# Kernel optimization log

Measured on AMD Instinct MI355X. Metric: run time of the kernel, lower is better.

## Reference

```python
import jax, jax.numpy as jnp
import numpy as np

B, N, C, H = 8, 1024, 768, 12
HD = C // H  # 64
SCALE = HD ** -0.5
T = 4
N_HALF = T // 2  # loop body with attention runs N_HALF times, V accumulates T times


def setup_inputs() -> dict:
    key = jax.random.key(0)
    ks = jax.random.split(key, 8)
    s = 0.02
    return {
        "x": jax.random.normal(ks[0], (B, N, C), jnp.float32),
        "Wqkv": jax.random.normal(ks[1], (3 * C, C), jnp.float32) * s,
        "Wfc1": jax.random.normal(ks[2], (HD, HD), jnp.float32) * s,
        "bfc1": jax.random.normal(ks[3], (HD,), jnp.float32) * s,
        "Wfc2": jax.random.normal(ks[4], (HD, HD), jnp.float32) * s,
        "bfc2": jax.random.normal(ks[5], (HD,), jnp.float32) * s,
        "Wproj": jax.random.normal(ks[6], (C, C), jnp.float32) * s,
        "bproj": jax.random.normal(ks[7], (C,), jnp.float32) * s,
    }


def reference(x, Wqkv, Wfc1, bfc1, Wfc2, bfc2, Wproj, bproj):
    b, n, c = x.shape
    # qkv projection (no bias), split into per-head q,k,v: [B,H,N,hd]
    qkv = (x @ Wqkv.T).reshape(b, n, 3, H, HD).transpose(2, 0, 3, 1, 4)
    q, k, v = qkv[0], qkv[1], qkv[2]
    # Loop body is stateless per timestep: first N_HALF steps each add the same
    # att_spk; all T steps add the same relu(v). Compute once, scale by counts.
    Q_spk = jax.nn.relu(q) @ Wfc1.T + bfc1  # [B,H,N,hd]
    K_spk = jax.nn.relu(k) @ Wfc2.T + bfc2  # [B,H,N,hd]
    att_spk = jax.nn.relu(jnp.einsum("bhqd,bhkd->bhqk", Q_spk, K_spk) * SCALE)
    att_rec = att_spk * float(N_HALF)   # accumulated over t < T/2
    V_rec = jax.nn.relu(v) * float(T)   # accumulated over all T steps
    att = jax.nn.softmax(att_rec, axis=-1)
    out = jnp.einsum("bhqk,bhkd->bhqd", att, V_rec)  # [B,H,N,hd]
    out = out.transpose(0, 2, 1, 3).reshape(b, n, c)
    return out @ Wproj.T + bproj
```

## Files before the change

### kernel.cpp

```cpp
#include <hip/hip_runtime.h>
#include <hip/hip_bf16.h>
#include <stdint.h>
#include <math.h>

#define BB   8
#define NN_  1024
#define CC   768
#define HH   12
#define HDD  64

typedef __attribute__((ext_vector_type(8))) short bf16x8;
typedef __attribute__((ext_vector_type(4))) float f32x4;
typedef __attribute__((ext_vector_type(16))) float f32x16;
typedef __attribute__((ext_vector_type(4))) float f32x4v;
typedef __attribute__((ext_vector_type(4))) unsigned short u16x4;

union FragU { unsigned int u[4]; bf16x8 b; };

__device__ __forceinline__ unsigned short f2bf(float f) {
    union { float f; unsigned int u; } v; v.f = f;
    unsigned int r = v.u + 0x7fffu + ((v.u >> 16) & 1u);
    return (unsigned short)(r >> 16);
}

#define CVTPK(d_, a_, b_) asm("v_cvt_pk_bf16_f32 %0, %1, %2" : "=v"(d_) : "v"(a_), "v"(b_))
#define SWAP32(a_, b_) asm("v_permlane32_swap_b32 %0, %1" : "+v"(a_), "+v"(b_))

#define GLDS(g_, l_) __builtin_amdgcn_global_load_lds( \
    (const __attribute__((address_space(1))) void*)(g_), \
    (__attribute__((address_space(3))) void*)(l_), 16, 0, 0)

#define MKFRAGS(P_, F0_, F1_) do {                                             \
    unsigned int c0,c1,c2,c3,c4,c5,c6,c7;                                      \
    CVTPK(c0, P_[0],  P_[1]);  CVTPK(c1, P_[2],  P_[3]);                       \
    CVTPK(c2, P_[4],  P_[5]);  CVTPK(c3, P_[6],  P_[7]);                       \
    CVTPK(c4, P_[8],  P_[9]);  CVTPK(c5, P_[10], P_[11]);                      \
    CVTPK(c6, P_[12], P_[13]); CVTPK(c7, P_[14], P_[15]);                      \
    SWAP32(c0, c2); SWAP32(c1, c3); SWAP32(c4, c6); SWAP32(c5, c7);            \
    FragU fu0_, fu1_;                                                          \
    fu0_.u[0]=c0; fu0_.u[1]=c1; fu0_.u[2]=c2; fu0_.u[3]=c3;                    \
    fu1_.u[0]=c4; fu1_.u[1]=c5; fu1_.u[2]=c6; fu1_.u[3]=c7;                    \
    F0_ = fu0_.b; F1_ = fu1_.b;                                                \
} while (0)

#define CVT_N0 1572864
#define CVT_N1 2015232
#define CVT_N2 2162688
#define CVT_N3 2163712
#define CVT_N4 2164736
__global__ void cvt_all(const float* __restrict__ x, const float* __restrict__ wqkv,
                        const float* __restrict__ wproj, const float* __restrict__ wf1,
                        const float* __restrict__ wf2,
                        unsigned short* __restrict__ xb, unsigned short* __restrict__ wqkvb,
                        unsigned short* __restrict__ wprojb, unsigned short* __restrict__ wf1b,
                        unsigned short* __restrict__ wf2b) {
    int i = blockIdx.x * blockDim.x + threadIdx.x;
    int stride = gridDim.x * blockDim.x;
    for (; i < CVT_N4; i += stride) {
        const f32x4v* src; u16x4* dst; int off;
        if (i < CVT_N0)      { src = (const f32x4v*)x;     dst = (u16x4*)xb;     off = i; }
        else if (i < CVT_N1) { src = (const f32x4v*)wqkv;  dst = (u16x4*)wqkvb;  off = i - CVT_N0; }
        else if (i < CVT_N2) { src = (const f32x4v*)wproj; dst = (u16x4*)wprojb; off = i - CVT_N1; }
        else if (i < CVT_N3) { src = (const f32x4v*)wf1;   dst = (u16x4*)wf1b;   off = i - CVT_N2; }
        else                 { src = (const f32x4v*)wf2;   dst = (u16x4*)wf2b;   off = i - CVT_N3; }
        f32x4v v = src[off];
        u16x4 o;
        o.x = f2bf(v.x); o.y = f2bf(v.y); o.z = f2bf(v.z); o.w = f2bf(v.w);
        dst[off] = o;
    }
}

__global__ __launch_bounds__(512, 1)
void qkv_spk_gemm(const unsigned short* __restrict__ X,
                  const unsigned short* __restrict__ Wqkv,
                  const unsigned short* __restrict__ Wf1,
                  const unsigned short* __restrict__ Wf2,
                  const float* __restrict__ bf1,
                  const float* __restrict__ bf2,
                  unsigned short* __restrict__ Rq,
                  unsigned short* __restrict__ Rk,
                  unsigned short* __restrict__ VT) {
    __shared__ short sA[4][8192];
    __shared__ short sB[4][4096];

    const int t    = threadIdx.x;
    const int wid  = t >> 6;
    const int lane = t & 63;
    const int l31  = lane & 31;
    const int hi5  = lane >> 5;
    const int fw   = wid >> 1;
    const int wn   = wid & 1;

    const int bid  = (int)blockIdx.x;
    const int c    = bid & 7;
    const int j    = bid >> 3;
    const int f_   = j % 9;
    const int g_   = j / 9;
    const int bx   = c * 8 + g_;
    const int by   = f_;
    const int F0   = by * 256;
    const int T0   = bx * 128;

#define STG(bi_, kt_) do {                                                     \
    _Pragma("unroll")                                                          \
    for (int i = 0; i < 2; i++) {                                              \
        int li_ = i * 512 + t;                                                 \
        int dr_ = li_ >> 3;                                                    \
        int u_  = (li_ & 7) ^ (dr_ & 7);                                       \
        GLDS(Wqkv + (size_t)(F0 + dr_ * 2 + (u_ >> 2)) * 768 + (kt_) * 32 + (u_ & 3) * 8, \
             &sA[bi_][li_ * 8]);                                               \
    }                                                                          \
    {                                                                          \
        int dr_ = t >> 3;                                                      \
        int u_  = (t & 7) ^ (dr_ & 7);                                         \
        GLDS(X + (size_t)(T0 + dr_ * 2 + (u_ >> 2)) * 768 + (kt_) * 32 + (u_ & 3) * 8, \
             &sB[bi_][t * 8]);                                                 \
    }                                                                          \
} while (0)

    f32x16 acc[2][2];
#pragma unroll
    for (int fb = 0; fb < 2; fb++)
#pragma unroll
        for (int tb = 0; tb < 2; tb++)
#pragma unroll
            for (int r = 0; r < 16; r++) acc[fb][tb][r] = 0.f;

    bf16x8 wA[2][2], xA[2][2], wB[2][2], xB[2][2];

#define RD(W_, X_, bc_) do {                                                   \
    const char* ab_ = (const char*)sA[bc_];                                    \
    const char* bb_ = (const char*)sB[bc_];                                    \
    _Pragma("unroll")                                                          \
    for (int fb = 0; fb < 2; fb++) {                                           \
        int r_ = fw * 64 + fb * 32 + l31;                                      \
        int dr_ = r_ >> 1;                                                     \
        _Pragma("unroll")                                                      \
        for (int ks = 0; ks < 2; ks++)                                         \
            W_[fb][ks] = *(const bf16x8*)(ab_ + dr_ * 128 +                    \
                ((((r_ & 1) * 4 + ks * 2 + hi5) ^ (dr_ & 7)) << 4));           \
    }                                                                          \
    _Pragma("unroll")                                                          \
    for (int tb = 0; tb < 2; tb++) {                                           \
        int r_ = wn * 64 + tb * 32 + l31;                                      \
        int dr_ = r_ >> 1;                                                     \
        _Pragma("unroll")                                                      \
        for (int ks = 0; ks < 2; ks++)                                         \
            X_[tb][ks] = *(const bf16x8*)(bb_ + dr_ * 128 +                    \
                ((((r_ & 1) * 4 + ks * 2 + hi5) ^ (dr_ & 7)) << 4));           \
    }                                                                          \
} while (0)

#define MFMA8(W_, X_)                                                          \
    _Pragma("unroll")                                                          \
    for (int ks = 0; ks < 2; ks++)                                             \
        _Pragma("unroll")                                                      \
        for (int fb = 0; fb < 2; fb++)                                         \
            _Pragma("unroll")                                                  \
            for (int tb = 0; tb < 2; tb++)                                     \
                acc[fb][tb] = __builtin_amdgcn_mfma_f32_32x32x16_bf16(         \
                    W_[fb][ks], X_[tb][ks], acc[fb][tb], 0, 0, 0)

#define PH(CW_, CX_, NW_, NX_, rb_, sb_, t_, VM_) do {                         \
    if ((t_) + 3 < 24) STG(sb_, (t_) + 3);                                     \
    asm volatile("s_waitcnt vmcnt(" #VM_ ")" ::: "memory");                    \
    __builtin_amdgcn_s_barrier();                                              \
    if ((t_) + 1 < 24) RD(NW_, NX_, rb_);                                      \
    __builtin_amdgcn_sched_barrier(0);                                         \
    __builtin_amdgcn_s_setprio(1);                                             \
    MFMA8(CW_, CX_);                                                           \
    __builtin_amdgcn_s_setprio(0);                                             \
    asm volatile("s_waitcnt lgkmcnt(0)" ::: "memory");                         \
} while (0)

    STG(0, 0); STG(1, 1); STG(2, 2);
    asm volatile("s_waitcnt vmcnt(6)" ::: "memory");
    __builtin_amdgcn_s_barrier();
    RD(wA, xA, 0);
    asm volatile("s_waitcnt lgkmcnt(0)" ::: "memory");

#pragma unroll 1
    for (int t4 = 0; t4 < 20; t4 += 4) {
        PH(wA, xA, wB, xB, 1, 3, t4 + 0, 6);
        PH(wB, xB, wA, xA, 2, 0, t4 + 1, 6);
        PH(wA, xA, wB, xB, 3, 1, t4 + 2, 6);
        PH(wB, xB, wA, xA, 0, 2, t4 + 3, 6);
    }
    PH(wA, xA, wB, xB, 1, 3, 20, 6);
    PH(wB, xB, wA, xA, 2, 0, 21, 3);
    PH(wA, xA, wB, xB, 3, 1, 22, 0);
    PH(wB, xB, wA, xA, 0, 2, 23, 0);
#undef PH
#undef MFMA8
#undef RD
#undef STG

    const int fbase = F0 + fw * 64;
    const int p  = fbase / 768;
    const int hh = (fbase - p * 768) >> 6;
    const int tok0 = T0 + wn * 64;
    const int b  = tok0 >> 10;
    const int n0 = tok0 & 1023;
    const int crow0 = 4 * hi5;

    if (p == 2) {
        const size_t vtb = ((size_t)(b * HH + hh)) * HDD * NN_;
#pragma unroll
        for (int fb = 0; fb < 2; fb++)
#pragma unroll
            for (int tb = 0; tb < 2; tb++)
#pragma unroll
                for (int r = 0; r < 16; r++) {
                    int d = fb * 32 + (r & 3) + 8 * (r >> 2) + crow0;
                    int n = n0 + tb * 32 + l31;
                    VT[vtb + (size_t)d * NN_ + n] = f2bf(4.f * fmaxf(acc[fb][tb][r], 0.f));
                }
    } else {
        const unsigned short* Wf = p ? Wf2 : Wf1;
        const float* bfp = p ? bf2 : bf1;
        unsigned short* R = p ? Rk : Rq;
        bf16x8 wfr[2][4];
#pragma unroll
        for (int dh = 0; dh < 2; dh++)
#pragma unroll
            for (int ks = 0; ks < 4; ks++)
                wfr[dh][ks] = *(const bf16x8*)&Wf[(size_t)(dh * 32 + l31) * HDD + ks * 16 + hi5 * 8];
        float bv0 = bfp[l31], bv1 = bfp[32 + l31];
        const size_t qkb = ((size_t)(b * HH + hh)) * NN_ * HDD;
#pragma unroll
        for (int tb = 0; tb < 2; tb++) {
            float pv0[16], pv1[16];
#pragma unroll
            for (int r = 0; r < 16; r++) {
                pv0[r] = fmaxf(acc[0][tb][r], 0.f);
                pv1[r] = fmaxf(acc[1][tb][r], 0.f);
            }
            bf16x8 pa0, pa1, pa2, pa3;
            MKFRAGS(pv0, pa0, pa1);
            MKFRAGS(pv1, pa2, pa3);
            f32x16 D0, D1;
#pragma unroll
            for (int r = 0; r < 16; r++) { D0[r] = 0.f; D1[r] = 0.f; }
            D0 = __builtin_amdgcn_mfma_f32_32x32x16_bf16(pa0, wfr[0][0], D0, 0, 0, 0);
            D0 = __builtin_amdgcn_mfma_f32_32x32x16_bf16(pa1, wfr[0][1], D0, 0, 0, 0);
            D0 = __builtin_amdgcn_mfma_f32_32x32x16_bf16(pa2, wfr[0][2], D0, 0, 0, 0);
            D0 = __builtin_amdgcn_mfma_f32_32x32x16_bf16(pa3, wfr[0][3], D0, 0, 0, 0);
            D1 = __builtin_amdgcn_mfma_f32_32x32x16_bf16(pa0, wfr[1][0], D1, 0, 0, 0);
            D1 = __builtin_amdgcn_mfma_f32_32x32x16_bf16(pa1, wfr[1][1], D1, 0, 0, 0);
            D1 = __builtin_amdgcn_mfma_f32_32x32x16_bf16(pa2, wfr[1][2], D1, 0, 0, 0);
            D1 = __builtin_amdgcn_mfma_f32_32x32x16_bf16(pa3, wfr[1][3], D1, 0, 0, 0);
#pragma unroll
            for (int r = 0; r < 16; r++) {
                int n = n0 + tb * 32 + (r & 3) + 8 * (r >> 2) + crow0;
                size_t rowb = qkb + (size_t)n * HDD;
                R[rowb + l31]      = f2bf(D0[r] + bv0);
                R[rowb + 32 + l31] = f2bf(D1[r] + bv1);
            }
        }
    }
}

__global__ __launch_bounds__(256, 2)
void attn_kernel(const unsigned short* __restrict__ Q,
                 const unsigned short* __restrict__ Kx,
                 const unsigned short* __restrict__ VT,
                 unsigned short* __restrict__ AO) {
    __shared__ short sK[2][64 * 64];
    __shared__ short sV[2][64 * 64];
    __shared__ float sinv[4][32];

    const int t    = threadIdx.x;
    const int lane = t & 63;
    const int wid  = t >> 6;
    const int l31  = lane & 31;
    const int hi5  = lane >> 5;

    const int bid = (int)blockIdx.x;
    const int lbid = (bid & 7) * 96 + (bid >> 3);
    const int bh = lbid >> 3;
    const int qt = lbid & 7;
    const int b = bh / HH, h = bh - b * HH;

    const unsigned short* Qs = Q  + (size_t)bh * NN_ * HDD;
    const unsigned short* Ks = Kx + (size_t)bh * NN_ * HDD;
    const unsigned short* Vt = VT + (size_t)bh * HDD * NN_;
    const int q0 = qt * 128 + wid * 32;

    bf16x8 qf[4];
#pragma unroll
    for (int ds = 0; ds < 4; ds++)
        qf[ds] = *(const bf16x8*)&Qs[(size_t)(q0 + l31) * HDD + ds * 16 + hi5 * 8];

    f32x16 O0, O1;
#pragma unroll
    for (int r = 0; r < 16; r++) { O0[r] = 0.f; O1[r] = 0.f; }
    float sumacc = 0.f;

    const int srow = t >> 3;
    const int sslot = t & 7;
    const int dstoff = ((t & 192)) * 8;

#define STAGE(buf_, kt_) do {                                                  \
    _Pragma("unroll")                                                          \
    for (int i = 0; i < 2; i++) {                                              \
        int row_ = srow + i * 32;                                              \
        int sl_  = (sslot ^ (row_ & 7)) << 3;                                  \
        const unsigned short* gk_ = Ks + (size_t)((kt_) * 64 + row_) * HDD + sl_; \
        const unsigned short* gv_ = Vt + (size_t)row_ * NN_ + (kt_) * 64 + sl_;   \
        GLDS(gk_, &sK[buf_][i * 2048 + dstoff]);                               \
        GLDS(gv_, &sV[buf_][i * 2048 + dstoff]);                               \
    }                                                                          \
} while (0)

    STAGE(0, 0);
    __syncthreads();

    int buf = 0;
    for (int kt = 0; kt < 16; ++kt) {
        if (kt < 15) STAGE(buf ^ 1, kt + 1);

        const char* kbase = (const char*)&sK[buf][0];
        const char* vbase = (const char*)&sV[buf][0];

        bf16x8 vbf[4][2];
#pragma unroll
        for (int ks = 0; ks < 4; ks++)
#pragma unroll
            for (int dt = 0; dt < 2; dt++) {
                int d = dt * 32 + l31;
                vbf[ks][dt] = *(const bf16x8*)(vbase + d * 128 +
                               ((ks * 32 + hi5 * 16) ^ ((d & 7) << 4)));
            }
        bf16x8 ka[2][4];
#pragma unroll
        for (int kt2 = 0; kt2 < 2; kt2++)
#pragma unroll
            for (int ds = 0; ds < 4; ds++) {
                int kk = kt2 * 32 + l31;
                ka[kt2][ds] = *(const bf16x8*)(kbase + kk * 128 +
                               ((ds * 32 + hi5 * 16) ^ ((kk & 7) << 4)));
            }

        f32x16 S0, S1;
#pragma unroll
        for (int r = 0; r < 16; r++) { S0[r] = 0.f; S1[r] = 0.f; }
#pragma unroll
        for (int ds = 0; ds < 4; ds++) {
            S0 = __builtin_amdgcn_mfma_f32_32x32x16_bf16(ka[0][ds], qf[ds], S0, 0, 0, 0);
            S1 = __builtin_amdgcn_mfma_f32_32x32x16_bf16(ka[1][ds], qf[ds], S1, 0, 0, 0);
        }

        float p0[16], p1[16];
#pragma unroll
        for (int r = 0; r < 16; r++) {
            p0[r] = exp2f(0.36067376f * fmaxf(S0[r], 0.f));
            p1[r] = exp2f(0.36067376f * fmaxf(S1[r], 0.f));
        }
        float s0 = 0.f, s1 = 0.f;
#pragma unroll
        for (int r = 0; r < 16; r++) { s0 += p0[r]; s1 += p1[r]; }
        sumacc += s0 + s1;

        bf16x8 paf0, paf1, paf2, paf3;
        MKFRAGS(p0, paf0, paf1);
        MKFRAGS(p1, paf2, paf3);

        O0 = __builtin_amdgcn_mfma_f32_32x32x16_bf16(paf0, vbf[0][0], O0, 0, 0, 0);
        O1 = __builtin_amdgcn_mfma_f32_32x32x16_bf16(paf0, vbf[0][1], O1, 0, 0, 0);
        O0 = __builtin_amdgcn_mfma_f32_32x32x16_bf16(paf1, vbf[1][0], O0, 0, 0, 0);
        O1 = __builtin_amdgcn_mfma_f32_32x32x16_bf16(paf1, vbf[1][1], O1, 0, 0, 0);
        O0 = __builtin_amdgcn_mfma_f32_32x32x16_bf16(paf2, vbf[2][0], O0, 0, 0, 0);
        O1 = __builtin_amdgcn_mfma_f32_32x32x16_bf16(paf2, vbf[2][1], O1, 0, 0, 0);
        O0 = __builtin_amdgcn_mfma_f32_32x32x16_bf16(paf3, vbf[3][0], O0, 0, 0, 0);
        O1 = __builtin_amdgcn_mfma_f32_32x32x16_bf16(paf3, vbf[3][1], O1, 0, 0, 0);

        __syncthreads();
        buf ^= 1;
    }
#undef STAGE

    float stot = sumacc + __shfl_xor(sumacc, 32, 64);
    float inv = 1.f / stot;
    if (l31 == lane) sinv[wid][l31] = inv;
    __syncthreads();

#pragma unroll
    for (int r = 0; r < 16; r++) {
        int qloc = (r & 3) + 8 * (r >> 2) + 4 * hi5;
        float iv = sinv[wid][qloc];
        size_t row = (size_t)(b * NN_ + q0 + qloc) * CC + h * HDD;
        AO[row + l31]      = f2bf(O0[r] * iv);
        AO[row + 32 + l31] = f2bf(O1[r] * iv);
    }
}

__global__ __launch_bounds__(256)
void proj_gemm(const unsigned short* __restrict__ A,
               const unsigned short* __restrict__ Bt,
               const float* __restrict__ bias,
               float* __restrict__ Out) {
    __shared__ short sA[128 * 32];
    __shared__ short sB[128 * 32];
    const int K = 768;
    const int lane = threadIdx.x & 63;
    const int wid  = threadIdx.x >> 6;
    const int wr = wid >> 1, wc = wid & 1;
    const int brow = blockIdx.x * 128;
    const int bcol = blockIdx.y * 128;
    const int t = threadIdx.x;

    f32x4 acc[4][4];
#pragma unroll
    for (int m = 0; m < 4; m++)
#pragma unroll
        for (int n = 0; n < 4; n++) acc[m][n] = (f32x4){0.f, 0.f, 0.f, 0.f};

    for (int k0 = 0; k0 < K; k0 += 32) {
#pragma unroll
        for (int i = 0; i < 2; i++) {
            int tt  = i * 256 + t;
            int row = tt >> 2;
            int kc  = (tt & 3) * 8;
            const unsigned short* ga = A  + (size_t)(brow + row) * K + k0 + kc;
            const unsigned short* gb = Bt + (size_t)(bcol + row) * K + k0 + kc;
            GLDS(ga, &sA[(i * 256 + wid * 64) * 8]);
            GLDS(gb, &sB[(i * 256 + wid * 64) * 8]);
        }
        __syncthreads();
        bf16x8 af[4], bfg[4];
#pragma unroll
        for (int m = 0; m < 4; m++) {
            int r = wr * 64 + m * 16 + (lane & 15);
            af[m] = *(const bf16x8*)&sA[r * 32 + (lane >> 4) * 8];
        }
#pragma unroll
        for (int n = 0; n < 4; n++) {
            int c = wc * 64 + n * 16 + (lane & 15);
            bfg[n] = *(const bf16x8*)&sB[c * 32 + (lane >> 4) * 8];
        }
#pragma unroll
        for (int m = 0; m < 4; m++)
#pragma unroll
            for (int n = 0; n < 4; n++)
                acc[m][n] = __builtin_amdgcn_mfma_f32_16x16x32_bf16(af[m], bfg[n], acc[m][n], 0, 0, 0);
        __syncthreads();
    }
#pragma unroll
    for (int m = 0; m < 4; m++)
#pragma unroll
        for (int n = 0; n < 4; n++) {
            int col = bcol + wc * 64 + n * 16 + (lane & 15);
            float bv = bias[col];
#pragma unroll
            for (int r = 0; r < 4; r++) {
                int row = brow + wr * 64 + m * 16 + (lane >> 4) * 4 + r;
                Out[(size_t)row * 768 + col] = acc[m][n][r] + bv;
            }
        }
}

extern "C" void kernel_launch(void* const* d_in, const int* in_sizes, int n_in,
                              void* d_out, int out_size, void* d_ws, size_t ws_size,
                              hipStream_t stream) {
    const float* x     = (const float*)d_in[0];
    const float* Wqkv  = (const float*)d_in[1];
    const float* Wfc1  = (const float*)d_in[2];
    const float* bfc1  = (const float*)d_in[3];
    const float* Wfc2  = (const float*)d_in[4];
    const float* bfc2  = (const float*)d_in[5];
    const float* Wproj = (const float*)d_in[6];
    const float* bproj = (const float*)d_in[7];
    float* out = (float*)d_out;

    char* ws = (char*)d_ws;
    const size_t SZ_XN = (size_t)8192 * 768 * 2;
    unsigned short* x_bf    = (unsigned short*)ws; ws += SZ_XN;
    unsigned short* wqkv_bf = (unsigned short*)ws; ws += (size_t)2304 * 768 * 2;
    unsigned short* wproj_bf= (unsigned short*)ws; ws += (size_t)768 * 768 * 2;
    unsigned short* wfc1_bf = (unsigned short*)ws; ws += 64 * 64 * 2;
    unsigned short* wfc2_bf = (unsigned short*)ws; ws += 64 * 64 * 2;
    unsigned short* Rq      = (unsigned short*)ws; ws += SZ_XN;
    unsigned short* Rk      = (unsigned short*)ws; ws += SZ_XN;
    unsigned short* VT      = (unsigned short*)ws; ws += SZ_XN;

    cvt_all<<<2048, 256, 0, stream>>>(x, Wqkv, Wproj, Wfc1, Wfc2,
                                      x_bf, wqkv_bf, wproj_bf, wfc1_bf, wfc2_bf);
    qkv_spk_gemm<<<576, 512, 0, stream>>>(x_bf, wqkv_bf, wfc1_bf, wfc2_bf,
                                          bfc1, bfc2, Rq, Rk, VT);
    attn_kernel<<<768, 256, 0, stream>>>(Rq, Rk, VT, x_bf);
    proj_gemm<<<dim3(64, 6), 256, 0, stream>>>(x_bf, wproj_bf, bproj, out);
}
```

Baseline: 134.8 us.

## Triple-buffer attention and proj loads; stream X fragments directly from global

The QKV GEMM stops staging X tiles through LDS. Each wave now loads its X fragments straight from global memory into registers two k-steps ahead, which frees LDS, and the launch-bounds occupancy hint is raised. The attention and projection kernels move from double-buffered loops with two __syncthreads per step to 3-stage buffers with prefetch two tiles ahead and one explicit vmcnt-wait plus barrier per step. The aim is more load/compute overlap and less synchronisation, at the cost of more registers and uncoalesced direct global reads of X.

Result: slower. 235.5 us (+74.7%).

```diff
diff --git a/kernel.cpp b/kernel.cpp
--- a/kernel.cpp
+++ b/kernel.cpp
@@ -70,8 +70,8 @@
     }
 }
 
-__global__ __launch_bounds__(512, 1)
-void qkv_spk_gemm(const unsigned short* __restrict__ X,
+__global__ __launch_bounds__(512, 4)
+void qkv_spk_gemm(const unsigned short* __restrict__ Xg,
                   const unsigned short* __restrict__ Wqkv,
                   const unsigned short* __restrict__ Wf1,
                   const unsigned short* __restrict__ Wf2,
@@ -81,7 +81,6 @@
                   unsigned short* __restrict__ Rk,
                   unsigned short* __restrict__ VT) {
     __shared__ short sA[4][8192];
-    __shared__ short sB[4][4096];
 
     const int t    = threadIdx.x;
     const int wid  = t >> 6;
@@ -101,7 +100,10 @@
     const int F0   = by * 256;
     const int T0   = bx * 128;
 
-#define STG(bi_, kt_) do {                                                     \
+    const int xrow = T0 + wn * 64 + l31;
+    const int xcol8 = hi5 * 8;
+
+#define STGA(bi_, kt_) do {                                                    \
     _Pragma("unroll")                                                          \
     for (int i = 0; i < 2; i++) {                                              \
         int li_ = i * 512 + t;                                                 \
@@ -110,12 +112,15 @@
         GLDS(Wqkv + (size_t)(F0 + dr_ * 2 + (u_ >> 2)) * 768 + (kt_) * 32 + (u_ & 3) * 8, \
              &sA[bi_][li_ * 8]);                                               \
     }                                                                          \
-    {                                                                          \
-        int dr_ = t >> 3;                                                      \
-        int u_  = (t & 7) ^ (dr_ & 7);                                         \
-        GLDS(X + (size_t)(T0 + dr_ * 2 + (u_ >> 2)) * 768 + (kt_) * 32 + (u_ & 3) * 8, \
-             &sB[bi_][t * 8]);                                                 \
-    }                                                                          \
+} while (0)
+
+#define XLD(X_, kt_) do {                                                      \
+    _Pragma("unroll")                                                          \
+    for (int tb = 0; tb < 2; tb++)                                             \
+        _Pragma("unroll")                                                      \
+        for (int ks = 0; ks < 2; ks++)                                         \
+            X_[tb][ks] = *(const bf16x8*)&Xg[(size_t)(xrow + tb * 32) * 768 +  \
+                                             (kt_) * 32 + ks * 16 + xcol8];    \
 } while (0)
 
     f32x16 acc[2][2];
@@ -126,11 +131,10 @@
 #pragma unroll
             for (int r = 0; r < 16; r++) acc[fb][tb][r] = 0.f;
 
-    bf16x8 wA[2][2], xA[2][2], wB[2][2], xB[2][2];
-
-#define RD(W_, X_, bc_) do {                                                   \
+    bf16x8 wA[2][2], wB[2][2], xA[2][2], xB[2][2];
+
+#define RDA(W_, bc_) do {                                                      \
     const char* ab_ = (const char*)sA[bc_];                                    \
-    const char* bb_ = (const char*)sB[bc_];                                    \
     _Pragma("unroll")                                                          \
     for (int fb = 0; fb < 2; fb++) {                                           \
         int r_ = fw * 64 + fb * 32 + l31;                                      \
@@ -140,15 +144,6 @@
             W_[fb][ks] = *(const bf16x8*)(ab_ + dr_ * 128 +                    \
                 ((((r_ & 1) * 4 + ks * 2 + hi5) ^ (dr_ & 7)) << 4));           \
     }                                                                          \
-    _Pragma("unroll")                                                          \
-    for (int tb = 0; tb < 2; tb++) {                                           \
-        int r_ = wn * 64 + tb * 32 + l31;                                      \
-        int dr_ = r_ >> 1;                                                     \
-        _Pragma("unroll")                                                      \
-        for (int ks = 0; ks < 2; ks++)                                         \
-            X_[tb][ks] = *(const bf16x8*)(bb_ + dr_ * 128 +                    \
-                ((((r_ & 1) * 4 + ks * 2 + hi5) ^ (dr_ & 7)) << 4));           \
-    }                                                                          \
 } while (0)
 
 #define MFMA8(W_, X_)                                                          \
@@ -161,39 +156,42 @@
                 acc[fb][tb] = __builtin_amdgcn_mfma_f32_32x32x16_bf16(         \
                     W_[fb][ks], X_[tb][ks], acc[fb][tb], 0, 0, 0)
 
-#define PH(CW_, CX_, NW_, NX_, rb_, sb_, t_, VM_) do {                         \
-    if ((t_) + 3 < 24) STG(sb_, (t_) + 3);                                     \
+#define PH(CW_, CX_, NW_, rb_, sb_, t_, VM_) do {                              \
+    if ((t_) + 3 < 24) STGA(sb_, (t_) + 3);                                    \
     asm volatile("s_waitcnt vmcnt(" #VM_ ")" ::: "memory");                    \
     __builtin_amdgcn_s_barrier();                                              \
-    if ((t_) + 1 < 24) RD(NW_, NX_, rb_);                                      \
+    if ((t_) + 1 < 24) RDA(NW_, rb_);                                          \
     __builtin_amdgcn_sched_barrier(0);                                         \
     __builtin_amdgcn_s_setprio(1);                                             \
     MFMA8(CW_, CX_);                                                           \
     __builtin_amdgcn_s_setprio(0);                                             \
+    if ((t_) + 2 < 24) XLD(CX_, (t_) + 2);                                     \
     asm volatile("s_waitcnt lgkmcnt(0)" ::: "memory");                         \
 } while (0)
 
-    STG(0, 0); STG(1, 1); STG(2, 2);
-    asm volatile("s_waitcnt vmcnt(6)" ::: "memory");
+    STGA(0, 0); STGA(1, 1); STGA(2, 2);
+    XLD(xA, 0); XLD(xB, 1);
+    asm volatile("s_waitcnt vmcnt(4)" ::: "memory");
     __builtin_amdgcn_s_barrier();
-    RD(wA, xA, 0);
+    RDA(wA, 0);
     asm volatile("s_waitcnt lgkmcnt(0)" ::: "memory");
 
 #pragma unroll 1
     for (int t4 = 0; t4 < 20; t4 += 4) {
-        PH(wA, xA, wB, xB, 1, 3, t4 + 0, 6);
-        PH(wB, xB, wA, xA, 2, 0, t4 + 1, 6);
-        PH(wA, xA, wB, xB, 3, 1, t4 + 2, 6);
-        PH(wB, xB, wA, xA, 0, 2, t4 + 3, 6);
+        PH(wA, xA, wB, 1, 3, t4 + 0, 8);
+        PH(wB, xB, wA, 2, 0, t4 + 1, 8);
+        PH(wA, xA, wB, 3, 1, t4 + 2, 8);
+        PH(wB, xB, wA, 0, 2, t4 + 3, 8);
     }
-    PH(wA, xA, wB, xB, 1, 3, 20, 6);
-    PH(wB, xB, wA, xA, 2, 0, 21, 3);
-    PH(wA, xA, wB, xB, 3, 1, 22, 0);
-    PH(wB, xB, wA, xA, 0, 2, 23, 0);
+    PH(wA, xA, wB, 1, 3, 20, 8);
+    PH(wB, xB, wA, 2, 0, 21, 6);
+    PH(wA, xA, wB, 3, 1, 22, 4);
+    PH(wB, xB, wA, 0, 2, 23, 0);
 #undef PH
 #undef MFMA8
-#undef RD
-#undef STG
+#undef RDA
+#undef XLD
+#undef STGA
 
     const int fbase = F0 + fw * 64;
     const int p  = fbase / 768;
@@ -265,8 +263,8 @@
                  const unsigned short* __restrict__ Kx,
                  const unsigned short* __restrict__ VT,
                  unsigned short* __restrict__ AO) {
-    __shared__ short sK[2][64 * 64];
-    __shared__ short sV[2][64 * 64];
+    __shared__ short sK[3][4096];
+    __shared__ short sV[3][4096];
     __shared__ float sinv[4][32];
 
     const int t    = threadIdx.x;
@@ -312,71 +310,76 @@
     }                                                                          \
 } while (0)
 
-    STAGE(0, 0);
-    __syncthreads();
-
-    int buf = 0;
-    for (int kt = 0; kt < 16; ++kt) {
-        if (kt < 15) STAGE(buf ^ 1, kt + 1);
-
-        const char* kbase = (const char*)&sK[buf][0];
-        const char* vbase = (const char*)&sV[buf][0];
-
-        bf16x8 vbf[4][2];
-#pragma unroll
-        for (int ks = 0; ks < 4; ks++)
-#pragma unroll
-            for (int dt = 0; dt < 2; dt++) {
-                int d = dt * 32 + l31;
-                vbf[ks][dt] = *(const bf16x8*)(vbase + d * 128 +
-                               ((ks * 32 + hi5 * 16) ^ ((d & 7) << 4)));
-            }
-        bf16x8 ka[2][4];
-#pragma unroll
-        for (int kt2 = 0; kt2 < 2; kt2++)
-#pragma unroll
-            for (int ds = 0; ds < 4; ds++) {
-                int kk = kt2 * 32 + l31;
-                ka[kt2][ds] = *(const bf16x8*)(kbase + kk * 128 +
-                               ((ds * 32 + hi5 * 16) ^ ((kk & 7) << 4)));
-            }
-
-        f32x16 S0, S1;
-#pragma unroll
-        for (int r = 0; r < 16; r++) { S0[r] = 0.f; S1[r] = 0.f; }
-#pragma unroll
-        for (int ds = 0; ds < 4; ds++) {
-            S0 = __builtin_amdgcn_mfma_f32_32x32x16_bf16(ka[0][ds], qf[ds], S0, 0, 0, 0);
-            S1 = __builtin_amdgcn_mfma_f32_32x32x16_bf16(ka[1][ds], qf[ds], S1, 0, 0, 0);
-        }
-
-        float p0[16], p1[16];
-#pragma unroll
-        for (int r = 0; r < 16; r++) {
-            p0[r] = exp2f(0.36067376f * fmaxf(S0[r], 0.f));
-            p1[r] = exp2f(0.36067376f * fmaxf(S1[r], 0.f));
-        }
-        float s0 = 0.f, s1 = 0.f;
-#pragma unroll
-        for (int r = 0; r < 16; r++) { s0 += p0[r]; s1 += p1[r]; }
-        sumacc += s0 + s1;
-
-        bf16x8 paf0, paf1, paf2, paf3;
-        MKFRAGS(p0, paf0, paf1);
-        MKFRAGS(p1, paf2, paf3);
-
-        O0 = __builtin_amdgcn_mfma_f32_32x32x16_bf16(paf0, vbf[0][0], O0, 0, 0, 0);
-        O1 = __builtin_amdgcn_mfma_f32_32x32x16_bf16(paf0, vbf[0][1], O1, 0, 0, 0);
-        O0 = __builtin_amdgcn_mfma_f32_32x32x16_bf16(paf1, vbf[1][0], O0, 0, 0, 0);
-        O1 = __builtin_amdgcn_mfma_f32_32x32x16_bf16(paf1, vbf[1][1], O1, 0, 0, 0);
-        O0 = __builtin_amdgcn_mfma_f32_32x32x16_bf16(paf2, vbf[2][0], O0, 0, 0, 0);
-        O1 = __builtin_amdgcn_mfma_f32_32x32x16_bf16(paf2, vbf[2][1], O1, 0, 0, 0);
-        O0 = __builtin_amdgcn_mfma_f32_32x32x16_bf16(paf3, vbf[3][0], O0, 0, 0, 0);
-        O1 = __builtin_amdgcn_mfma_f32_32x32x16_bf16(paf3, vbf[3][1], O1, 0, 0, 0);
-
-        __syncthreads();
-        buf ^= 1;
+#define ABODY(cb_, sb_, kt_, VM_) do {                                         \
+    if ((kt_) + 2 < 16) STAGE(sb_, (kt_) + 2);                                 \
+    const char* kbase = (const char*)&sK[cb_][0];                              \
+    const char* vbase = (const char*)&sV[cb_][0];                              \
+    bf16x8 vbf[4][2];                                                          \
+    _Pragma("unroll")                                                          \
+    for (int ks = 0; ks < 4; ks++)                                             \
+        _Pragma("unroll")                                                      \
+        for (int dt = 0; dt < 2; dt++) {                                       \
+            int d = dt * 32 + l31;                                             \
+            vbf[ks][dt] = *(const bf16x8*)(vbase + d * 128 +                   \
+                           ((ks * 32 + hi5 * 16) ^ ((d & 7) << 4)));           \
+        }                                                                      \
+    bf16x8 ka[2][4];                                                           \
+    _Pragma("unroll")                                                          \
+    for (int kt2 = 0; kt2 < 2; kt2++)                                          \
+        _Pragma("unroll")                                                      \
+        for (int ds = 0; ds < 4; ds++) {                                       \
+            int kk = kt2 * 32 + l31;                                           \
+            ka[kt2][ds] = *(const bf16x8*)(kbase + kk * 128 +                  \
+                           ((ds * 32 + hi5 * 16) ^ ((kk & 7) << 4)));          \
+        }                                                                      \
+    f32x16 S0, S1;                                                             \
+    _Pragma("unroll")                                                          \
+    for (int r = 0; r < 16; r++) { S0[r] = 0.f; S1[r] = 0.f; }                 \
+    _Pragma("unroll")                                                          \
+    for (int ds = 0; ds < 4; ds++) {                                           \
+        S0 = __builtin_amdgcn_mfma_f32_32x32x16_bf16(ka[0][ds], qf[ds], S0, 0, 0, 0); \
+        S1 = __builtin_amdgcn_mfma_f32_32x32x16_bf16(ka[1][ds], qf[ds], S1, 0, 0, 0); \
+    }                                                                          \
+    float p0[16], p1[16];                                                      \
+    _Pragma("unroll")                                                          \
+    for (int r = 0; r < 16; r++) {                                             \
+        p0[r] = exp2f(0.36067376f * fmaxf(S0[r], 0.f));                        \
+        p1[r] = exp2f(0.36067376f * fmaxf(S1[r], 0.f));                        \
+    }                                                                          \
+    float s0 = 0.f, s1 = 0.f;                                                  \
+    _Pragma("unroll")                                                          \
+    for (int r = 0; r < 16; r++) { s0 += p0[r]; s1 += p1[r]; }                 \
+    sumacc += s0 + s1;                                                         \
+    bf16x8 paf0, paf1, paf2, paf3;                                             \
+    MKFRAGS(p0, paf0, paf1);                                                   \
+    MKFRAGS(p1, paf2, paf3);                                                   \
+    O0 = __builtin_amdgcn_mfma_f32_32x32x16_bf16(paf0, vbf[0][0], O0, 0, 0, 0);\
+    O1 = __builtin_amdgcn_mfma_f32_32x32x16_bf16(paf0, vbf[0][1], O1, 0, 0, 0);\
+    O0 = __builtin_amdgcn_mfma_f32_32x32x16_bf16(paf1, vbf[1][0], O0, 0, 0, 0);\
+    O1 = __builtin_amdgcn_mfma_f32_32x32x16_bf16(paf1, vbf[1][1], O1, 0, 0, 0);\
+    O0 = __builtin_amdgcn_mfma_f32_32x32x16_bf16(paf2, vbf[2][0], O0, 0, 0, 0);\
+    O1 = __builtin_amdgcn_mfma_f32_32x32x16_bf16(paf2, vbf[2][1], O1, 0, 0, 0);\
+    O0 = __builtin_amdgcn_mfma_f32_32x32x16_bf16(paf3, vbf[3][0], O0, 0, 0, 0);\
+    O1 = __builtin_amdgcn_mfma_f32_32x32x16_bf16(paf3, vbf[3][1], O1, 0, 0, 0);\
+    asm volatile("s_waitcnt vmcnt(" #VM_ ")" ::: "memory");                    \
+    __builtin_amdgcn_s_barrier();                                              \
+} while (0)
+
+    STAGE(0, 0); STAGE(1, 1);
+    asm volatile("s_waitcnt vmcnt(4)" ::: "memory");
+    __builtin_amdgcn_s_barrier();
+
+#pragma unroll 1
+    for (int kt3 = 0; kt3 < 12; kt3 += 3) {
+        ABODY(0, 2, kt3 + 0, 4);
+        ABODY(1, 0, kt3 + 1, 4);
+        ABODY(2, 1, kt3 + 2, 4);
     }
+    ABODY(0, 2, 12, 4);
+    ABODY(1, 0, 13, 4);
+    ABODY(2, 1, 14, 0);
+    ABODY(0, 2, 15, 0);
+#undef ABODY
 #undef STAGE
 
     float stot = sumacc + __shfl_xor(sumacc, 32, 64);
@@ -399,8 +402,8 @@
                const unsigned short* __restrict__ Bt,
                const float* __restrict__ bias,
                float* __restrict__ Out) {
-    __shared__ short sA[128 * 32];
-    __shared__ short sB[128 * 32];
+    __shared__ short sA[3][4096];
+    __shared__ short sB[3][4096];
     const int K = 768;
     const int lane = threadIdx.x & 63;
     const int wid  = threadIdx.x >> 6;
@@ -415,36 +418,57 @@
 #pragma unroll
         for (int n = 0; n < 4; n++) acc[m][n] = (f32x4){0.f, 0.f, 0.f, 0.f};
 
-    for (int k0 = 0; k0 < K; k0 += 32) {
-#pragma unroll
-        for (int i = 0; i < 2; i++) {
-            int tt  = i * 256 + t;
-            int row = tt >> 2;
-            int kc  = (tt & 3) * 8;
-            const unsigned short* ga = A  + (size_t)(brow + row) * K + k0 + kc;
-            const unsigned short* gb = Bt + (size_t)(bcol + row) * K + k0 + kc;
-            GLDS(ga, &sA[(i * 256 + wid * 64) * 8]);
-            GLDS(gb, &sB[(i * 256 + wid * 64) * 8]);
-        }
-        __syncthreads();
-        bf16x8 af[4], bfg[4];
-#pragma unroll
-        for (int m = 0; m < 4; m++) {
-            int r = wr * 64 + m * 16 + (lane & 15);
-            af[m] = *(const bf16x8*)&sA[r * 32 + (lane >> 4) * 8];
-        }
-#pragma unroll
-        for (int n = 0; n < 4; n++) {
-            int c = wc * 64 + n * 16 + (lane & 15);
-            bfg[n] = *(const bf16x8*)&sB[c * 32 + (lane >> 4) * 8];
-        }
-#pragma unroll
-        for (int m = 0; m < 4; m++)
-#pragma unroll
-            for (int n = 0; n < 4; n++)
-                acc[m][n] = __builtin_amdgcn_mfma_f32_16x16x32_bf16(af[m], bfg[n], acc[m][n], 0, 0, 0);
-        __syncthreads();
+#define PSTG(buf_, kt_) do {                                                   \
+    _Pragma("unroll")                                                          \
+    for (int i = 0; i < 2; i++) {                                              \
+        int tt  = i * 256 + t;                                                 \
+        int row = tt >> 2;                                                     \
+        int kc  = (tt & 3) * 8;                                                \
+        GLDS(A  + (size_t)(brow + row) * K + (kt_) * 32 + kc,                  \
+             &sA[buf_][(i * 256 + wid * 64) * 8]);                             \
+        GLDS(Bt + (size_t)(bcol + row) * K + (kt_) * 32 + kc,                  \
+             &sB[buf_][(i * 256 + wid * 64) * 8]);                             \
+    }                                                                          \
+} while (0)
+
+#define PBODY(cb_, sb_, kt_, VM_) do {                                         \
+    if ((kt_) + 2 < 24) PSTG(sb_, (kt_) + 2);                                  \
+    bf16x8 af[4], bfg[4];                                                      \
+    _Pragma("unroll")                                                          \
+    for (int m = 0; m < 4; m++) {                                              \
+        int r = wr * 64 + m * 16 + (lane & 15);                                \
+        af[m] = *(const bf16x8*)&sA[cb_][r * 32 + (lane >> 4) * 8];            \
+    }                                                                          \
+    _Pragma("unroll")                                                          \
+    for (int n = 0; n < 4; n++) {                                              \
+        int cc2 = wc * 64 + n * 16 + (lane & 15);                              \
+        bfg[n] = *(const bf16x8*)&sB[cb_][cc2 * 32 + (lane >> 4) * 8];         \
+    }                                                                          \
+    _Pragma("unroll")                                                          \
+    for (int m = 0; m < 4; m++)                                                \
+        _Pragma("unroll")                                                      \
+        for (int n = 0; n < 4; n++)                                            \
+            acc[m][n] = __builtin_amdgcn_mfma_f32_16x16x32_bf16(af[m], bfg[n], acc[m][n], 0, 0, 0); \
+    asm volatile("s_waitcnt vmcnt(" #VM_ ")" ::: "memory");                    \
+    __builtin_amdgcn_s_barrier();                                              \
+} while (0)
+
+    PSTG(0, 0); PSTG(1, 1);
+    asm volatile("s_waitcnt vmcnt(4)" ::: "memory");
+    __builtin_amdgcn_s_barrier();
+
+#pragma unroll 1
+    for (int kt3 = 0; kt3 < 21; kt3 += 3) {
+        PBODY(0, 2, kt3 + 0, 4);
+        PBODY(1, 0, kt3 + 1, 4);
+        PBODY(2, 1, kt3 + 2, 4);
     }
+    PBODY(0, 2, 21, 4);
+    PBODY(1, 0, 22, 0);
+    PBODY(2, 1, 23, 0);
+#undef PBODY
+#undef PSTG
+
 #pragma unroll
     for (int m = 0; m < 4; m++)
 #pragma unroll
```
